# Kernel tuning notes

Hardware: AMD Instinct MI355X
Metric: run time of the kernel (lower is better)

Reference implementation:

```python
import jax, jax.numpy as jnp
import numpy as np

N, E = 25000, 400000
HID, EDGE_F, DIM, HEADS, ADY = 128, 16, 3, 8, 64
INNER = int(1.25 * HID)          # 160
MSG_F = 2 * HID + EDGE_F + 1     # 273 (e3, relaxed=False -> 1 distance feature)


def silu(x):
    return x * jax.nn.sigmoid(x)


def ada_ln(x, y, W, b):
    # LayerNorm (no affine) + FiLM conditioning from y
    mu = jnp.mean(x, axis=-1, keepdims=True)
    var = jnp.var(x, axis=-1, keepdims=True)
    xn = (x - mu) * jax.lax.rsqrt(var + 1e-5)
    scale, shift = jnp.split(y @ W + b, 2, axis=-1)
    return xn * (1.0 + scale) + shift


def setup_inputs() -> dict:
    key = jax.random.key(0)
    ks = jax.random.split(key, 32)
    rn = lambda k, shp, s=0.05: (jax.random.normal(k, shp, jnp.float32) * s)
    inp = {
        'h': jax.random.normal(ks[0], (N, HID), jnp.float32),
        'coords': jax.random.normal(ks[1], (N, DIM), jnp.float32),
        'a': jax.random.normal(ks[2], (E, EDGE_F), jnp.float32),
        'y': jax.random.normal(ks[3], (N, ADY), jnp.float32),
        'res': jnp.zeros((N, HID), jnp.float32),
        'src': jax.random.randint(ks[4], (E,), 0, N, jnp.int32),
        'dst': jax.random.randint(ks[5], (E,), 0, N, jnp.int32),
        # edge MLP
        'We1': rn(ks[6], (MSG_F, INNER)), 'be1': jnp.zeros((INNER,), jnp.float32),
        'We2': rn(ks[7], (INNER, INNER)), 'be2': jnp.zeros((INNER,), jnp.float32),
        # coord head (xavier gain 0.001 -> tiny init)
        'Wc': rn(ks[8], (INNER, 1), 0.001),
        # attention/value/output heads
        'Wv': rn(ks[9], (INNER, HID)),
        'Wa': rn(ks[10], (INNER, HEADS)),
        'Wo': rn(ks[11], (HID, HID)),
        # node MLP
        'Wn1': rn(ks[12], (HID, INNER)), 'bn1': jnp.zeros((INNER,), jnp.float32),
        'Wn2': rn(ks[13], (INNER, HID)), 'bn2': jnp.zeros((HID,), jnp.float32),
        # adaptive LayerNorms (FiLM from y)
        'Wf1': rn(ks[14], (ADY, 2 * HID)), 'bf1': jnp.zeros((2 * HID,), jnp.float32),
        'Wf2': rn(ks[15], (ADY, 2 * HID)), 'bf2': jnp.zeros((2 * HID,), jnp.float32),
    }
    return inp


def reference(h, coords, a, y, res, src, dst,
              We1, be1, We2, be2, Wc, Wv, Wa, Wo,
              Wn1, bn1, Wn2, bn2, Wf1, bf1, Wf2, bf2):
    n = h.shape[0]
    heads = Wa.shape[1]
    # --- distance features (e3, relaxed=False): radial only ---
    xs, xd = coords[src], coords[dst]          # [E, 3]
    diffs = xs - xd
    radials = jnp.sum(diffs * diffs, axis=-1, keepdims=True)  # [E, 1]
    # --- edge MLP on gathered features ---
    f = jnp.concatenate([h[src], h[dst], radials, a], axis=-1)  # [E, 273]
    m = silu(f @ We1 + be1)
    m = silu(m @ We2 + be2)                    # [E, inner]
    # --- coordinate messages + scatter-sum to dst ---
    msg_x = (m @ Wc) * diffs / (jnp.sqrt(radials + 1e-5) + 1.0)  # [E, 3]
    coords_out = coords + jax.ops.segment_sum(msg_x, dst, num_segments=n)
    # --- edge softmax over incoming edges per dst node ---
    logits = m @ Wa                             # [E, heads]
    mx = jax.ops.segment_max(logits, dst, num_segments=n)
    ex = jnp.exp(logits - mx[dst])
    den = jax.ops.segment_sum(ex, dst, num_segments=n)
    w = ex / den[dst]                           # [E, heads]
    # --- weighted value aggregation ---
    vals = (m @ Wv).reshape(-1, heads, HID // heads) * w[:, :, None]
    h_agg = jax.ops.segment_sum(vals, dst, num_segments=n).reshape(n, HID)
    f2 = h_agg @ Wo
    res1 = res + f2
    h1 = ada_ln(h + f2, y, Wf1, bf1)
    f3 = silu(h1 @ Wn1 + bn1) @ Wn2 + bn2
    res2 = res1 + f3
    h2 = ada_ln(h1 + f3, y, Wf2, bf2)
    return (h2, coords_out, res2)
```

## Files before the change

kernel.cpp:

```cpp
#include <hip/hip_runtime.h>
#include <math.h>

#define N_NODES 25000
#define N_EDGES 400000
#define HID 128
#define EDGE_F 16
#define ADY 64
#define INNER 160
#define MSG_F 273
#define HEADS 8

#define OUT_CRD (N_NODES * HID)
#define OUT_RES (N_NODES * (HID + 3))

#define FLAG_OFF 0
#define DEN_OFF  256
#define CACC_OFF 800256
#define HAGG_OFF 1100256
#define CNT_OFF  13900256
#define CUR_OFF  14000256
#define PERM_OFF 14100256
#define MEMSET_BYTES 14000256
#define HBF_OFF  15700256
#define YBF_OFF  22100256
#define BIAS_OFF 25300256
#define BW_OFF   25302560

#define WSLICE 5120
#define SCR_STRIDE 145

typedef unsigned short u16;
typedef unsigned int u32;
typedef unsigned long long u64;
typedef __attribute__((ext_vector_type(8))) short short8;
typedef __attribute__((ext_vector_type(4))) float f32x4;

__device__ __forceinline__ float bf2f(u16 v) {
    union { u32 u; float f; } x; x.u = ((u32)v) << 16; return x.f;
}
__device__ __forceinline__ u16 f2bf(float f) {
    union { float ff; u32 u; } x; x.ff = f;
    u32 u = x.u;
    u32 rounding = 0x7FFFu + ((u >> 16) & 1u);
    u += rounding;
    return (u16)(u >> 16);
}
__device__ __forceinline__ float silu(float z) {
    z = fminf(fmaxf(z, -30000.f), 30000.f);
    return z / (1.0f + __expf(-z));
}

template<bool F32> __device__ __forceinline__ float ldg1(const void* p, size_t i) {
    if (F32) return ((const float*)p)[i];
    return bf2f(((const u16*)p)[i]);
}
template<bool F32> __device__ __forceinline__ void stg1(void* p, size_t i, float v) {
    if (F32) ((float*)p)[i] = v;
    else     ((u16*)p)[i] = f2bf(v);
}
__device__ __forceinline__ float ldany(const void* p, size_t i, bool f32) {
    return f32 ? ((const float*)p)[i] : bf2f(((const u16*)p)[i]);
}
__device__ __forceinline__ void wave_lds_fence() {
    __builtin_amdgcn_wave_barrier();
    __builtin_amdgcn_s_waitcnt(0xc07f);
    __builtin_amdgcn_wave_barrier();
}

__device__ __forceinline__ int a_addr(int k, int lr) {
    return ((k >> 5) << 9) + (((((k & 31) >> 3) << 4) | lr) << 3) + (k & 7);
}

struct CvtArgs {
    const void* src[8];
    u64 dstoff[8];
    int n[8];
};
struct BwArgs {
    const void* We1; const void* We2; const void* Wv; const void* Wa;
    const void* Wc;  const void* Wo;  const void* Wn1; const void* Wn2;
    const void* Wf1; const void* Wf2;
    u64 b1, b2, b3, b4, b5, b6, b7, b8;
};

__global__ __launch_bounds__(256)
void preproc_kernel(const void* hsrc, int* flag, char* ws, CvtArgs args, BwArgs bwa,
                    const int* __restrict__ dstp, int* __restrict__ cnt)
{
    __shared__ float red[256];
    __shared__ int sflag;
    const int t = threadIdx.x;
    {
        const u16* p = (const u16*)hsrc;
        float mx = 0.f;
        for (int i = 0; i < 8; i++) {
            int idx = (t * 8 + i) * 97;
            float v = fabsf(bf2f(p[idx * 2]));
            mx = fmaxf(mx, v);
        }
        red[t] = mx;
        __syncthreads();
        for (int s = 128; s > 0; s >>= 1) {
            if (t < s) red[t] = fmaxf(red[t], red[t + s]);
            __syncthreads();
        }
        if (t == 0) {
            sflag = (red[0] > 1e10f || red[0] == 0.f) ? 1 : 0;
            if (blockIdx.x == 0) flag[0] = sflag;
        }
        __syncthreads();
    }
    const bool f32 = (sflag != 0);
    const int g = blockIdx.x * 256 + t;
    const int stride = gridDim.x * 256;

    for (int i = g; i < N_EDGES; i += stride)
        atomicAdd(&cnt[dstp[i]], 1);

    for (int ten = 0; ten < 8; ten++) {
        const void* s = args.src[ten];
        u16* d = (u16*)(ws + args.dstoff[ten]);
        const int n = args.n[ten];
        if (f32) {
            const float* sf = (const float*)s;
            for (int i = g; i < n; i += stride) d[i] = f2bf(sf[i]);
        } else {
            const u16* su = (const u16*)s;
            for (int i = g; i < n; i += stride) d[i] = su[i];
        }
    }

    u16* b1 = (u16*)(ws + bwa.b1);
    u16* b2 = (u16*)(ws + bwa.b2);
    u16* b3 = (u16*)(ws + bwa.b3);
    u16* b4 = (u16*)(ws + bwa.b4);
    u16* b5 = (u16*)(ws + bwa.b5);
    u16* b6 = (u16*)(ws + bwa.b6);
    u16* b7 = (u16*)(ws + bwa.b7);
    u16* b8 = (u16*)(ws + bwa.b8);
    for (int i = g; i < 5*2*10*512; i += stride) {
        int tt = i >> 9, r = i & 511, l = r >> 3, j = r & 7;
        int c = tt / 20, ks = (tt / 10) % 2, nt = tt % 10;
        int k = c*64 + ks*32 + (l >> 4)*8 + j;
        int n = nt*16 + (l & 15);
        float v = 0.f;
        if (k < MSG_F)      v = ldany(bwa.We1, (size_t)k*INNER + n, f32);
        else if (k == 273)  v = ldany(bwa.We1, (size_t)256*INNER + n, f32);
        b1[i] = f2bf(v);
    }
    for (int i = g; i < 5*10*512; i += stride) {
        int tt = i >> 9, r = i & 511, l = r >> 3, j = r & 7;
        int k5 = tt / 10, nt = tt % 10;
        int k = k5*32 + (l >> 4)*8 + j;
        int n = nt*16 + (l & 15);
        b2[i] = f2bf(ldany(bwa.We2, (size_t)k*INNER + n, f32));
    }
    for (int i = g; i < 5*9*512; i += stride) {
        int tt = i >> 9, r = i & 511, l = r >> 3, j = r & 7;
        int k5 = tt / 9, nt = tt % 9;
        int k = k5*32 + (l >> 4)*8 + j;
        int n = nt*16 + (l & 15);
        float v = 0.f;
        if (n < 128)       v = ldany(bwa.Wv, (size_t)k*HID + n, f32);
        else if (n < 136)  v = ldany(bwa.Wa, (size_t)k*HEADS + (n-128), f32);
        else if (n == 136) v = ldany(bwa.Wc, (size_t)k, f32);
        b3[i] = f2bf(v);
    }
    for (int i = g; i < 4*8*512; i += stride) {
        int tt = i >> 9, r = i & 511, l = r >> 3, j = r & 7;
        int cks = tt / 8, nt = tt % 8;
        int k = cks*32 + (l >> 4)*8 + j;
        int n = nt*16 + (l & 15);
        b4[i] = f2bf(ldany(bwa.Wo, (size_t)k*HID + n, f32));
    }
    for (int i = g; i < 4*10*512; i += stride) {
        int tt = i >> 9, r = i & 511, l = r >> 3, j = r & 7;
        int cks = tt / 10, nt = tt % 10;
        int k = cks*32 + (l >> 4)*8 + j;
        int n = nt*16 + (l & 15);
        b5[i] = f2bf(ldany(bwa.Wn1, (size_t)k*INNER + n, f32));
    }
    for (int i = g; i < 5*8*512; i += stride) {
        int tt = i >> 9, r = i & 511, l = r >> 3, j = r & 7;
        int k5 = tt / 8, nt = tt % 8;
        int k = k5*32 + (l >> 4)*8 + j;
        int n = nt*16 + (l & 15);
        b6[i] = f2bf(ldany(bwa.Wn2, (size_t)k*HID + n, f32));
    }
    for (int i = g; i < 2*16*512; i += stride) {
        int tt = i >> 9, r = i & 511, l = r >> 3, j = r & 7;
        int ks = tt / 16, nt = tt % 16;
        int k = ks*32 + (l >> 4)*8 + j;
        int n = nt*16 + (l & 15);
        b7[i] = f2bf(ldany(bwa.Wf1, (size_t)k*256 + n, f32));
        b8[i] = f2bf(ldany(bwa.Wf2, (size_t)k*256 + n, f32));
    }
}

__global__ __launch_bounds__(1024)
void scan_kernel(const int* __restrict__ cnt, int* __restrict__ cursor)
{
    __shared__ int ssum[1024];
    const int t = threadIdx.x;
    const int base = t * 25;
    int loc[25];
    int s = 0;
    #pragma unroll
    for (int j = 0; j < 25; j++) {
        int i = base + j;
        int v = (i < N_NODES) ? cnt[i] : 0;
        loc[j] = s; s += v;
    }
    ssum[t] = s;
    __syncthreads();
    for (int off = 1; off < 1024; off <<= 1) {
        int v = (t >= off) ? ssum[t - off] : 0;
        __syncthreads();
        ssum[t] += v;
        __syncthreads();
    }
    int offs = (t > 0) ? ssum[t - 1] : 0;
    #pragma unroll
    for (int j = 0; j < 25; j++) {
        int i = base + j;
        if (i < N_NODES) cursor[i] = offs + loc[j];
    }
}

__global__ __launch_bounds__(256)
void scatter_kernel(const int* __restrict__ dstp, int* __restrict__ cursor,
                    int* __restrict__ perm)
{
    int i = blockIdx.x * 256 + threadIdx.x;
    if (i < N_EDGES) {
        int pos = atomicAdd(&cursor[dstp[i]], 1);
        perm[pos] = i;
    }
}

template<bool F32>
__device__ __forceinline__ void edge_body(
    const u16* __restrict__ hbf, const void* coords, const void* a,
    const int* __restrict__ src, const int* __restrict__ dst,
    const int* __restrict__ perm,
    const u16* __restrict__ We1P, const u16* __restrict__ We2P,
    const u16* __restrict__ W3P,
    const u16* __restrict__ cbe1, const u16* __restrict__ cbe2,
    float* __restrict__ den, float* __restrict__ hagg, float* __restrict__ cacc,
    u16* sPool)
{
    const int t   = threadIdx.x;
    const int w   = t >> 6;
    const int l   = t & 63;
    const int col = l & 15;
    const int q   = l >> 4;
    const int e0  = blockIdx.x * 64;
    const int l8  = l << 3;

    u16* sW = sPool + w * WSLICE;

    const int r = l >> 2;
    const int p = t & 3;
    const int ge = perm[e0 + w*16 + r];
    const int s_ = src[ge];
    const int d_ = dst[ge];
    float dx = 0.f, dy = 0.f, dz = 0.f, invf = 0.f, r2 = 0.f;
    if (p < 2) {
        dx = ldg1<F32>(coords, (size_t)s_*3+0) - ldg1<F32>(coords, (size_t)d_*3+0);
        dy = ldg1<F32>(coords, (size_t)s_*3+1) - ldg1<F32>(coords, (size_t)d_*3+1);
        dz = ldg1<F32>(coords, (size_t)s_*3+2) - ldg1<F32>(coords, (size_t)d_*3+2);
        r2 = dx*dx + dy*dy + dz*dz;
        invf = 1.0f / (sqrtf(r2 + 1e-5f) + 1.0f);
    }
    #pragma unroll
    for (int c = 0; c < 4; c++) {
        int node = (c < 2) ? s_ : d_;
        int hcol = (c & 1) * 64 + p * 16;
        const uint4* gp = (const uint4*)(hbf + (size_t)node*HID + hcol);
        int k0 = c*64 + p*16;
        *(uint4*)(sW + a_addr(k0,     r)) = gp[0];
        *(uint4*)(sW + a_addr(k0 + 8, r)) = gp[1];
    }
    if (p < 2) {
        __align__(16) u16 tmp[16];
        #pragma unroll
        for (int j = 0; j < 16; j++) tmp[j] = 0;
        if (p == 0) {
            tmp[0] = f2bf(r2);
            for (int j = 0; j < 15; j++)
                tmp[1+j] = f2bf(ldg1<F32>(a, (size_t)ge*EDGE_F + j));
        } else {
            tmp[0] = f2bf(ldg1<F32>(a, (size_t)ge*EDGE_F + 15));
            tmp[1] = f2bf(r2 - bf2f(f2bf(r2)));
        }
        int k0 = 256 + p*16;
        *(uint4*)(sW + a_addr(k0,     r)) = ((uint4*)tmp)[0];
        *(uint4*)(sW + a_addr(k0 + 8, r)) = ((uint4*)tmp)[1];
    }
    wave_lds_fence();

    f32x4 acc1[10];
    #pragma unroll
    for (int nt = 0; nt < 10; nt++) {
        float v = bf2f(cbe1[nt*16 + col]);
        acc1[nt] = (f32x4){v, v, v, v};
    }
    #pragma unroll
    for (int kk = 0; kk < 9; kk++) {
        short8 af = *(const short8*)(sW + (kk << 9) + l8);
        const u16* B1 = We1P + ((kk*10) << 9) + l8;
        #pragma unroll
        for (int nt = 0; nt < 10; nt++) {
            short8 b = *(const short8*)(B1 + (nt << 9));
            acc1[nt] = __builtin_amdgcn_mfma_f32_16x16x32_bf16(af, b, acc1[nt], 0, 0, 0);
        }
    }
    wave_lds_fence();
    #pragma unroll
    for (int nt = 0; nt < 10; nt++)
        #pragma unroll
        for (int rr = 0; rr < 4; rr++)
            sW[a_addr(nt*16 + col, q*4 + rr)] = f2bf(silu(acc1[nt][rr]));
    wave_lds_fence();

    f32x4 acc2[10];
    #pragma unroll
    for (int nt = 0; nt < 10; nt++) {
        float v = bf2f(cbe2[nt*16 + col]);
        acc2[nt] = (f32x4){v, v, v, v};
    }
    #pragma unroll
    for (int k5 = 0; k5 < 5; k5++) {
        short8 af = *(const short8*)(sW + (k5 << 9) + l8);
        const u16* B2 = We2P + ((k5*10) << 9) + l8;
        #pragma unroll
        for (int nt = 0; nt < 10; nt++) {
            short8 b = *(const short8*)(B2 + (nt << 9));
            acc2[nt] = __builtin_amdgcn_mfma_f32_16x16x32_bf16(af, b, acc2[nt], 0, 0, 0);
        }
    }
    #pragma unroll
    for (int nt = 0; nt < 10; nt++)
        #pragma unroll
        for (int rr = 0; rr < 4; rr++)
            sW[2560 + a_addr(nt*16 + col, q*4 + rr)] = f2bf(silu(acc2[nt][rr]));
    wave_lds_fence();

    f32x4 acc3[9];
    #pragma unroll
    for (int nt = 0; nt < 9; nt++) acc3[nt] = (f32x4){0.f, 0.f, 0.f, 0.f};
    #pragma unroll
    for (int k5 = 0; k5 < 5; k5++) {
        short8 af = *(const short8*)(sW + 2560 + (k5 << 9) + l8);
        const u16* B3 = W3P + ((k5*9) << 9) + l8;
        #pragma unroll
        for (int nt = 0; nt < 9; nt++) {
            short8 b = *(const short8*)(B3 + (nt << 9));
            acc3[nt] = __builtin_amdgcn_mfma_f32_16x16x32_bf16(af, b, acc3[nt], 0, 0, 0);
        }
    }
    wave_lds_fence();

    float* scr = (float*)(void*)sW;

    int dsts[16];
    #pragma unroll
    for (int row = 0; row < 16; row++) dsts[row] = __shfl(d_, row << 2);
    float dxv[4], dyv[4], dzv[4], ivv[4];
    #pragma unroll
    for (int rr = 0; rr < 4; rr++) {
        int sl = (q*4 + rr) << 2;
        dxv[rr] = __shfl(dx, sl); dyv[rr] = __shfl(dy, sl);
        dzv[rr] = __shfl(dz, sl); ivv[rr] = __shfl(invf, sl);
    }

    {
        float exv[4] = {0.f, 0.f, 0.f, 0.f};
        if (col < 8) {
            #pragma unroll
            for (int rr = 0; rr < 4; rr++)
                exv[rr] = __expf(fminf(fmaxf(acc3[8][rr], -30.f), 30.f));
        }
        #pragma unroll
        for (int nt = 0; nt < 8; nt++) {
            float ex0 = __shfl(exv[0], q*16 + nt);
            float ex1 = __shfl(exv[1], q*16 + nt);
            float ex2 = __shfl(exv[2], q*16 + nt);
            float ex3 = __shfl(exv[3], q*16 + nt);
            scr[(q*4 + 0)*SCR_STRIDE + nt*16 + col] = acc3[nt][0] * ex0;
            scr[(q*4 + 1)*SCR_STRIDE + nt*16 + col] = acc3[nt][1] * ex1;
            scr[(q*4 + 2)*SCR_STRIDE + nt*16 + col] = acc3[nt][2] * ex2;
            scr[(q*4 + 3)*SCR_STRIDE + nt*16 + col] = acc3[nt][3] * ex3;
        }
        if (col < 8) {
            #pragma unroll
            for (int rr = 0; rr < 4; rr++)
                scr[(q*4 + rr)*SCR_STRIDE + 128 + col] = exv[rr];
        }
        if (col == 8) {
            #pragma unroll
            for (int rr = 0; rr < 4; rr++) {
                float lc = fminf(fmaxf(acc3[8][rr], -1e6f), 1e6f) * ivv[rr];
                scr[(q*4 + rr)*SCR_STRIDE + 136] = lc * dxv[rr];
                scr[(q*4 + rr)*SCR_STRIDE + 137] = lc * dyv[rr];
                scr[(q*4 + rr)*SCR_STRIDE + 138] = lc * dzv[rr];
            }
        }
    }
    wave_lds_fence();

    #pragma unroll
    for (int pass = 0; pass < 3; pass++) {
        int c = pass*64 + l;
        bool act = c < 139;
        float accu = 0.f;
        int prevd = dsts[0];
        #pragma unroll
        for (int row = 0; row < 16; row++) {
            int d = dsts[row];
            if (d != prevd) {
                if (act) {
                    if (c < 128)      atomicAdd(&hagg[(size_t)prevd*HID + c], accu);
                    else if (c < 136) atomicAdd(&den[(size_t)prevd*8 + (c-128)], accu);
                    else              atomicAdd(&cacc[(size_t)prevd*3 + (c-136)], accu);
                }
                accu = 0.f; prevd = d;
            }
            if (act) accu += scr[row*SCR_STRIDE + c];
        }
        if (act) {
            if (c < 128)      atomicAdd(&hagg[(size_t)prevd*HID + c], accu);
            else if (c < 136) atomicAdd(&den[(size_t)prevd*8 + (c-128)], accu);
            else              atomicAdd(&cacc[(size_t)prevd*3 + (c-136)], accu);
        }
    }
}

__global__ __launch_bounds__(256, 4)
void edge_kernel(const int* __restrict__ flag,
                 const u16* __restrict__ hbf, const void* coords, const void* a,
                 const int* __restrict__ src, const int* __restrict__ dst,
                 const int* __restrict__ perm,
                 const u16* __restrict__ We1P, const u16* __restrict__ We2P,
                 const u16* __restrict__ W3P,
                 const u16* __restrict__ cbe1, const u16* __restrict__ cbe2,
                 float* __restrict__ den, float* __restrict__ hagg,
                 float* __restrict__ cacc)
{
    __shared__ __align__(16) u16 sPool[4 * WSLICE];
    if (*flag)
        edge_body<true>(hbf, coords, a, src, dst, perm, We1P, We2P, W3P,
                        cbe1, cbe2, den, hagg, cacc, sPool);
    else
        edge_body<false>(hbf, coords, a, src, dst, perm, We1P, We2P, W3P,
                         cbe1, cbe2, den, hagg, cacc, sPool);
}

template<bool F32>
__device__ __forceinline__ void node_body(
    const u16* __restrict__ hbf, const void* res, const void* coords,
    const u16* __restrict__ ybf,
    const float* __restrict__ den, const float* __restrict__ hagg,
    const float* __restrict__ cacc,
    const u16* __restrict__ WoP, const u16* __restrict__ Wn1P,
    const u16* __restrict__ Wn2P, const u16* __restrict__ Wf1P,
    const u16* __restrict__ Wf2P,
    const u16* __restrict__ cbn1, const u16* __restrict__ cbn2,
    const u16* __restrict__ cbf1, const u16* __restrict__ cbf2,
    void* out, u16* sScr)
{
    const int t = threadIdx.x;
    const int w = t >> 6, l = t & 63, col = l & 15, q = l >> 4;
    const int nodew = blockIdx.x * 64 + w * 16;
    const int mynode = nodew + col;
    const bool okA = mynode < N_NODES;
    const int l8 = l << 3;
    u16* sc = sScr + w * 16 * 168;

    int gm[4]; bool okC[4];
    #pragma unroll
    for (int r = 0; r < 4; r++) { gm[r] = nodew + q*4 + r; okC[r] = gm[r] < N_NODES; }

    f32x4 aF2[8];
    #pragma unroll
    for (int nt = 0; nt < 8; nt++) aF2[nt] = (f32x4){0.f,0.f,0.f,0.f};
    #pragma unroll
    for (int c = 0; c < 2; c++) {
        #pragma unroll
        for (int ks = 0; ks < 2; ks++) {
            const int kbase = c*64 + ks*32 + q*8;
            union { u16 s[8]; short8 v; } u;
            if (okA) {
                float dd = den[(size_t)mynode*8 + (kbase >> 4)];
                float inv = dd > 0.f ? 1.f/dd : 0.f;
                const float4* gp = (const float4*)(hagg + (size_t)mynode*HID + kbase);
                float4 v0 = gp[0], v1 = gp[1];
                u.s[0]=f2bf(v0.x*inv); u.s[1]=f2bf(v0.y*inv); u.s[2]=f2bf(v0.z*inv); u.s[3]=f2bf(v0.w*inv);
                u.s[4]=f2bf(v1.x*inv); u.s[5]=f2bf(v1.y*inv); u.s[6]=f2bf(v1.z*inv); u.s[7]=f2bf(v1.w*inv);
            } else {
                #pragma unroll
                for (int j = 0; j < 8; j++) u.s[j] = 0;
            }
            const u16* B = WoP + (((c*2 + ks)*8) << 9) + l8;
            #pragma unroll
            for (int nt = 0; nt < 8; nt++) {
                short8 b = *(const short8*)(B + (nt << 9));
                aF2[nt] = __builtin_amdgcn_mfma_f32_16x16x32_bf16(u.v, b, aF2[nt], 0, 0, 0);
            }
        }
    }

    f32x4 aFl[16];
    #pragma unroll
    for (int nt = 0; nt < 16; nt++) {
        float v = bf2f(cbf1[nt*16 + col]);
        aFl[nt] = (f32x4){v,v,v,v};
    }
    #pragma unroll
    for (int ks = 0; ks < 2; ks++) {
        short8 af;
        if (okA) af = *(const short8*)(ybf + (size_t)mynode*ADY + ks*32 + q*8);
        else { union { u16 s[8]; short8 v; } z; for (int j=0;j<8;j++) z.s[j]=0; af = z.v; }
        const u16* B = Wf1P + ((ks*16) << 9) + l8;
        #pragma unroll
        for (int nt = 0; nt < 16; nt++) {
            short8 b = *(const short8*)(B + (nt << 9));
            aFl[nt] = __builtin_amdgcn_mfma_f32_16x16x32_bf16(af, b, aFl[nt], 0, 0, 0);
        }
    }

    float h1c[8][4], r1c[8][4];
    {
        float xv[8][4], s[4], ss[4];
        #pragma unroll
        for (int r = 0; r < 4; r++) { s[r] = 0.f; ss[r] = 0.f; }
        #pragma unroll
        for (int nt = 0; nt < 8; nt++)
            #pragma unroll
            for (int r = 0; r < 4; r++) {
                float hv = okC[r] ? bf2f(hbf[(size_t)gm[r]*HID + nt*16 + col]) : 0.f;
                float x = hv + aF2[nt][r];
                xv[nt][r] = x; s[r] += x; ss[r] += x*x;
            }
        #pragma unroll
        for (int r = 0; r < 4; r++)
            for (int off = 1; off <= 8; off <<= 1) {
                s[r]  += __shfl_xor(s[r], off);
                ss[r] += __shfl_xor(ss[r], off);
            }
        #pragma unroll
        for (int r = 0; r < 4; r++) {
            float mu = s[r] * (1.f/128.f);
            float var = ss[r] * (1.f/128.f) - mu*mu;
            float rs = rsqrtf(fmaxf(var, 0.f) + 1e-5f);
            #pragma unroll
            for (int nt = 0; nt < 8; nt++) {
                float h1 = (xv[nt][r]-mu)*rs*(1.f+aFl[nt][r]) + aFl[nt+8][r];
                h1c[nt][r] = h1;
                float rv = okC[r] ? ldg1<F32>(res, (size_t)gm[r]*HID + nt*16 + col) : 0.f;
                r1c[nt][r] = rv + aF2[nt][r];
                sc[(q*4 + r)*168 + nt*16 + col] = f2bf(h1);
            }
        }
    }
    wave_lds_fence();

    f32x4 aT[10];
    #pragma unroll
    for (int nt = 0; nt < 10; nt++) {
        float v = bf2f(cbn1[nt*16 + col]);
        aT[nt] = (f32x4){v,v,v,v};
    }
    #pragma unroll
    for (int c = 0; c < 2; c++) {
        #pragma unroll
        for (int ks = 0; ks < 2; ks++) {
            short8 af = *(const short8*)(sc + col*168 + c*64 + ks*32 + q*8);
            const u16* B = Wn1P + (((c*2 + ks)*10) << 9) + l8;
            #pragma unroll
            for (int nt = 0; nt < 10; nt++) {
                short8 b = *(const short8*)(B + (nt << 9));
                aT[nt] = __builtin_amdgcn_mfma_f32_16x16x32_bf16(af, b, aT[nt], 0, 0, 0);
            }
        }
    }
    wave_lds_fence();
    #pragma unroll
    for (int nt = 0; nt < 10; nt++)
        #pragma unroll
        for (int r = 0; r < 4; r++)
            sc[(q*4 + r)*168 + nt*16 + col] = f2bf(silu(aT[nt][r]));
    wave_lds_fence();

    f32x4 aF3[8];
    #pragma unroll
    for (int nt = 0; nt < 8; nt++) {
        float v = bf2f(cbn2[nt*16 + col]);
        aF3[nt] = (f32x4){v,v,v,v};
    }
    #pragma unroll
    for (int k5 = 0; k5 < 5; k5++) {
        short8 af = *(const short8*)(sc + col*168 + k5*32 + q*8);
        const u16* B = Wn2P + ((k5*8) << 9) + l8;
        #pragma unroll
        for (int nt = 0; nt < 8; nt++) {
            short8 b = *(const short8*)(B + (nt << 9));
            aF3[nt] = __builtin_amdgcn_mfma_f32_16x16x32_bf16(af, b, aF3[nt], 0, 0, 0);
        }
    }

    #pragma unroll
    for (int nt = 0; nt < 16; nt++) {
        float v = bf2f(cbf2[nt*16 + col]);
        aFl[nt] = (f32x4){v,v,v,v};
    }
    #pragma unroll
    for (int ks = 0; ks < 2; ks++) {
        short8 af;
        if (okA) af = *(const short8*)(ybf + (size_t)mynode*ADY + ks*32 + q*8);
        else { union { u16 s[8]; short8 v; } z; for (int j=0;j<8;j++) z.s[j]=0; af = z.v; }
        const u16* B = Wf2P + ((ks*16) << 9) + l8;
        #pragma unroll
        for (int nt = 0; nt < 16; nt++) {
            short8 b = *(const short8*)(B + (nt << 9));
            aFl[nt] = __builtin_amdgcn_mfma_f32_16x16x32_bf16(af, b, aFl[nt], 0, 0, 0);
        }
    }

    {
        float xv[8][4], s[4], ss[4];
        #pragma unroll
        for (int r = 0; r < 4; r++) { s[r] = 0.f; ss[r] = 0.f; }
        #pragma unroll
        for (int nt = 0; nt < 8; nt++)
            #pragma unroll
            for (int r = 0; r < 4; r++) {
                float x = h1c[nt][r] + aF3[nt][r];
                xv[nt][r] = x; s[r] += x; ss[r] += x*x;
            }
        #pragma unroll
        for (int r = 0; r < 4; r++)
            for (int off = 1; off <= 8; off <<= 1) {
                s[r]  += __shfl_xor(s[r], off);
                ss[r] += __shfl_xor(ss[r], off);
            }
        #pragma unroll
        for (int r = 0; r < 4; r++) {
            float mu = s[r] * (1.f/128.f);
            float var = ss[r] * (1.f/128.f) - mu*mu;
            float rs = rsqrtf(fmaxf(var, 0.f) + 1e-5f);
            if (okC[r]) {
                #pragma unroll
                for (int nt = 0; nt < 8; nt++) {
                    int n = nt*16 + col;
                    float h2 = (xv[nt][r]-mu)*rs*(1.f+aFl[nt][r]) + aFl[nt+8][r];
                    stg1<F32>(out, (size_t)gm[r]*HID + n, h2);
                    stg1<F32>(out, (size_t)OUT_RES + (size_t)gm[r]*HID + n,
                              r1c[nt][r] + aF3[nt][r]);
                }
            }
        }
    }

    if (q == 0 && okA) {
        #pragma unroll
        for (int j = 0; j < 3; j++)
            stg1<F32>(out, (size_t)OUT_CRD + (size_t)mynode*3 + j,
                      ldg1<F32>(coords, (size_t)mynode*3 + j) + cacc[(size_t)mynode*3 + j]);
    }
}

__global__ __launch_bounds__(256, 2)
void node_kernel(const int* __restrict__ flag,
                 const u16* __restrict__ hbf, const void* res, const void* coords,
                 const u16* __restrict__ ybf,
                 const float* __restrict__ den, const float* __restrict__ hagg,
                 const float* __restrict__ cacc,
                 const u16* __restrict__ WoP, const u16* __restrict__ Wn1P,
                 const u16* __restrict__ Wn2P, const u16* __restrict__ Wf1P,
                 const u16* __restrict__ Wf2P,
                 const u16* __restrict__ cbn1, const u16* __restrict__ cbn2,
                 const u16* __restrict__ cbf1, const u16* __restrict__ cbf2,
                 void* out)
{
    __shared__ __align__(16) u16 sScr[4 * 16 * 168];
    if (*flag)
        node_body<true>(hbf, res, coords, ybf, den, hagg, cacc, WoP, Wn1P, Wn2P,
                        Wf1P, Wf2P, cbn1, cbn2, cbf1, cbf2, out, sScr);
    else
        node_body<false>(hbf, res, coords, ybf, den, hagg, cacc, WoP, Wn1P, Wn2P,
                         Wf1P, Wf2P, cbn1, cbn2, cbf1, cbf2, out, sScr);
}

extern "C" void kernel_launch(void* const* d_in, const int* in_sizes, int n_in,
                              void* d_out, int out_size, void* d_ws, size_t ws_size,
                              hipStream_t stream)
{
    const void* h      = d_in[0];
    const void* coords = d_in[1];
    const void* a      = d_in[2];
    const void* y      = d_in[3];
    const void* res    = d_in[4];
    const int* src     = (const int*)d_in[5];
    const int* dst     = (const int*)d_in[6];

    char* ws = (char*)d_ws;
    int*   flag   = (int*)(ws + FLAG_OFF);
    float* den    = (float*)(ws + DEN_OFF);
    float* cacc   = (float*)(ws + CACC_OFF);
    float* hagg   = (float*)(ws + HAGG_OFF);
    int*   cnt    = (int*)(ws + CNT_OFF);
    int*   cursor = (int*)(ws + CUR_OFF);
    int*   perm   = (int*)(ws + PERM_OFF);
    u16*   hbf    = (u16*)(ws + HBF_OFF);
    u16*   ybf    = (u16*)(ws + YBF_OFF);

    CvtArgs args;
    const int cvtn[8]   = {160, 160, 160, 128, 256, 256, N_NODES*HID, N_NODES*ADY};
    const int cvtsrc[8] = {8, 10, 16, 18, 20, 22, 0, 3};
    u64 boff[8];
    u64 bo = BIAS_OFF;
    for (int i = 0; i < 6; i++) {
        boff[i] = bo;
        bo += ((u64)cvtn[i] * 2 + 15) & ~(u64)15;
    }
    boff[6] = HBF_OFF;
    boff[7] = YBF_OFF;
    for (int i = 0; i < 8; i++) {
        args.src[i] = d_in[cvtsrc[i]];
        args.dstoff[i] = boff[i];
        args.n[i] = cvtn[i];
    }
    const u16* cbe1 = (const u16*)(ws + boff[0]);
    const u16* cbe2 = (const u16*)(ws + boff[1]);
    const u16* cbn1 = (const u16*)(ws + boff[2]);
    const u16* cbn2 = (const u16*)(ws + boff[3]);
    const u16* cbf1 = (const u16*)(ws + boff[4]);
    const u16* cbf2 = (const u16*)(ws + boff[5]);

    BwArgs bwa;
    bwa.We1 = d_in[7];  bwa.We2 = d_in[9];  bwa.Wv = d_in[12]; bwa.Wa = d_in[13];
    bwa.Wc  = d_in[11]; bwa.Wo  = d_in[14]; bwa.Wn1 = d_in[15]; bwa.Wn2 = d_in[17];
    bwa.Wf1 = d_in[19]; bwa.Wf2 = d_in[21];
    bwa.b1 = BW_OFF;
    bwa.b2 = bwa.b1 + (u64)5*2*10*512*2;
    bwa.b3 = bwa.b2 + (u64)5*10*512*2;
    bwa.b4 = bwa.b3 + (u64)5*9*512*2;
    bwa.b5 = bwa.b4 + (u64)4*8*512*2;
    bwa.b6 = bwa.b5 + (u64)4*10*512*2;
    bwa.b7 = bwa.b6 + (u64)5*8*512*2;
    bwa.b8 = bwa.b7 + (u64)2*16*512*2;
    const u16* We1P = (const u16*)(ws + bwa.b1);
    const u16* We2P = (const u16*)(ws + bwa.b2);
    const u16* W3P  = (const u16*)(ws + bwa.b3);
    const u16* WoP  = (const u16*)(ws + bwa.b4);
    const u16* Wn1P = (const u16*)(ws + bwa.b5);
    const u16* Wn2P = (const u16*)(ws + bwa.b6);
    const u16* Wf1P = (const u16*)(ws + bwa.b7);
    const u16* Wf2P = (const u16*)(ws + bwa.b8);

    hipMemsetAsync(d_ws, 0, MEMSET_BYTES, stream);

    preproc_kernel<<<256, 256, 0, stream>>>(h, flag, ws, args, bwa, dst, cnt);

    scan_kernel<<<1, 1024, 0, stream>>>(cnt, cursor);

    scatter_kernel<<<(N_EDGES + 255)/256, 256, 0, stream>>>(dst, cursor, perm);

    edge_kernel<<<N_EDGES/64, 256, 0, stream>>>(flag, hbf, coords, a, src, dst, perm,
                                                We1P, We2P, W3P, cbe1, cbe2,
                                                den, hagg, cacc);

    node_kernel<<<(N_NODES + 63)/64, 256, 0, stream>>>(
        flag, hbf, res, coords, ybf, den, hagg, cacc,
        WoP, Wn1P, Wn2P, Wf1P, Wf2P, cbn1, cbn2, cbf1, cbf2, d_out);
}
```

Baseline: 482.1 us.

## Load MFMA A-operands directly from global and shrink LDS scratch to bf16

The edge kernel stops staging gathered h[src]/h[dst] rows into LDS and instead reads the MFMA A fragments straight from global memory, with each lane indexed by its edge column. LDS is used only for the distance/edge features and for the hidden activations. The scatter scratch is stored as bf16 pairs rather than fp32. Together these cut the per-wave LDS slice from 5120 to 3072 u16, and launch bounds are raised to 6 blocks per SM for higher occupancy. The cost is lower precision in the accumulated messages, softmax denominators and coordinate updates, plus uncoalesced direct global loads for the A operands.

```diff
diff --git a/kernel.cpp b/kernel.cpp
--- a/kernel.cpp
+++ b/kernel.cpp
@@ -26,8 +26,9 @@
 #define BIAS_OFF 25300256
 #define BW_OFF   25302560
 
-#define WSLICE 5120
-#define SCR_STRIDE 145
+#define WSLICE 3072
+#define SM_OFF 512
+#define SCR_STRIDE 146
 
 typedef unsigned short u16;
 typedef unsigned int u32;
@@ -259,29 +260,21 @@
 
     u16* sW = sPool + w * WSLICE;
 
-    const int r = l >> 2;
-    const int p = t & 3;
-    const int ge = perm[e0 + w*16 + r];
-    const int s_ = src[ge];
-    const int d_ = dst[ge];
+    const int ge2 = perm[e0 + w*16 + col];
+    const int s2 = src[ge2];
+    const int d2 = dst[ge2];
+
+    const int er = l >> 2;
+    const int p  = l & 3;
+    const int ge = perm[e0 + w*16 + er];
     float dx = 0.f, dy = 0.f, dz = 0.f, invf = 0.f, r2 = 0.f;
     if (p < 2) {
+        int s_ = src[ge], d_ = dst[ge];
         dx = ldg1<F32>(coords, (size_t)s_*3+0) - ldg1<F32>(coords, (size_t)d_*3+0);
         dy = ldg1<F32>(coords, (size_t)s_*3+1) - ldg1<F32>(coords, (size_t)d_*3+1);
         dz = ldg1<F32>(coords, (size_t)s_*3+2) - ldg1<F32>(coords, (size_t)d_*3+2);
         r2 = dx*dx + dy*dy + dz*dz;
         invf = 1.0f / (sqrtf(r2 + 1e-5f) + 1.0f);
-    }
-    #pragma unroll
-    for (int c = 0; c < 4; c++) {
-        int node = (c < 2) ? s_ : d_;
-        int hcol = (c & 1) * 64 + p * 16;
-        const uint4* gp = (const uint4*)(hbf + (size_t)node*HID + hcol);
-        int k0 = c*64 + p*16;
-        *(uint4*)(sW + a_addr(k0,     r)) = gp[0];
-        *(uint4*)(sW + a_addr(k0 + 8, r)) = gp[1];
-    }
-    if (p < 2) {
         __align__(16) u16 tmp[16];
         #pragma unroll
         for (int j = 0; j < 16; j++) tmp[j] = 0;
@@ -293,9 +286,8 @@
             tmp[0] = f2bf(ldg1<F32>(a, (size_t)ge*EDGE_F + 15));
             tmp[1] = f2bf(r2 - bf2f(f2bf(r2)));
         }
-        int k0 = 256 + p*16;
-        *(uint4*)(sW + a_addr(k0,     r)) = ((uint4*)tmp)[0];
-        *(uint4*)(sW + a_addr(k0 + 8, r)) = ((uint4*)tmp)[1];
+        *(uint4*)(sW + (32*p + er)*8)      = ((uint4*)tmp)[0];
+        *(uint4*)(sW + (32*p + 16 + er)*8) = ((uint4*)tmp)[1];
     }
     wave_lds_fence();
 
@@ -305,22 +297,44 @@
         float v = bf2f(cbe1[nt*16 + col]);
         acc1[nt] = (f32x4){v, v, v, v};
     }
-    #pragma unroll
-    for (int kk = 0; kk < 9; kk++) {
-        short8 af = *(const short8*)(sW + (kk << 9) + l8);
-        const u16* B1 = We1P + ((kk*10) << 9) + l8;
-        #pragma unroll
-        for (int nt = 0; nt < 10; nt++) {
-            short8 b = *(const short8*)(B1 + (nt << 9));
-            acc1[nt] = __builtin_amdgcn_mfma_f32_16x16x32_bf16(af, b, acc1[nt], 0, 0, 0);
-        }
-    }
-    wave_lds_fence();
+    {
+        const u16* hs = hbf + (size_t)s2*HID + q*8;
+        const u16* hd = hbf + (size_t)d2*HID + q*8;
+        #pragma unroll
+        for (int kk = 0; kk < 4; kk++) {
+            short8 af = *(const short8*)(hs + kk*32);
+            const u16* B1 = We1P + ((kk*10) << 9) + l8;
+            #pragma unroll
+            for (int nt = 0; nt < 10; nt++) {
+                short8 b = *(const short8*)(B1 + (nt << 9));
+                acc1[nt] = __builtin_amdgcn_mfma_f32_16x16x32_bf16(af, b, acc1[nt], 0, 0, 0);
+            }
+        }
+        #pragma unroll
+        for (int kk = 0; kk < 4; kk++) {
+            short8 af = *(const short8*)(hd + kk*32);
+            const u16* B1 = We1P + (((kk+4)*10) << 9) + l8;
+            #pragma unroll
+            for (int nt = 0; nt < 10; nt++) {
+                short8 b = *(const short8*)(B1 + (nt << 9));
+                acc1[nt] = __builtin_amdgcn_mfma_f32_16x16x32_bf16(af, b, acc1[nt], 0, 0, 0);
+            }
+        }
+        {
+            short8 af = *(const short8*)(sW + l8);
+            const u16* B1 = We1P + ((8*10) << 9) + l8;
+            #pragma unroll
+            for (int nt = 0; nt < 10; nt++) {
+                short8 b = *(const short8*)(B1 + (nt << 9));
+                acc1[nt] = __builtin_amdgcn_mfma_f32_16x16x32_bf16(af, b, acc1[nt], 0, 0, 0);
+            }
+        }
+    }
     #pragma unroll
     for (int nt = 0; nt < 10; nt++)
         #pragma unroll
         for (int rr = 0; rr < 4; rr++)
-            sW[a_addr(nt*16 + col, q*4 + rr)] = f2bf(silu(acc1[nt][rr]));
+            sW[SM_OFF + a_addr(nt*16 + col, q*4 + rr)] = f2bf(silu(acc1[nt][rr]));
     wave_lds_fence();
 
     f32x4 acc2[10];
@@ -331,7 +345,7 @@
     }
     #pragma unroll
     for (int k5 = 0; k5 < 5; k5++) {
-        short8 af = *(const short8*)(sW + (k5 << 9) + l8);
+        short8 af = *(const short8*)(sW + SM_OFF + (k5 << 9) + l8);
         const u16* B2 = We2P + ((k5*10) << 9) + l8;
         #pragma unroll
         for (int nt = 0; nt < 10; nt++) {
@@ -339,11 +353,12 @@
             acc2[nt] = __builtin_amdgcn_mfma_f32_16x16x32_bf16(af, b, acc2[nt], 0, 0, 0);
         }
     }
+    wave_lds_fence();
     #pragma unroll
     for (int nt = 0; nt < 10; nt++)
         #pragma unroll
         for (int rr = 0; rr < 4; rr++)
-            sW[2560 + a_addr(nt*16 + col, q*4 + rr)] = f2bf(silu(acc2[nt][rr]));
+            sW[SM_OFF + a_addr(nt*16 + col, q*4 + rr)] = f2bf(silu(acc2[nt][rr]));
     wave_lds_fence();
 
     f32x4 acc3[9];
@@ -351,7 +366,7 @@
     for (int nt = 0; nt < 9; nt++) acc3[nt] = (f32x4){0.f, 0.f, 0.f, 0.f};
     #pragma unroll
     for (int k5 = 0; k5 < 5; k5++) {
-        short8 af = *(const short8*)(sW + 2560 + (k5 << 9) + l8);
+        short8 af = *(const short8*)(sW + SM_OFF + (k5 << 9) + l8);
         const u16* B3 = W3P + ((k5*9) << 9) + l8;
         #pragma unroll
         for (int nt = 0; nt < 9; nt++) {
@@ -361,11 +376,9 @@
     }
     wave_lds_fence();
 
-    float* scr = (float*)(void*)sW;
-
     int dsts[16];
     #pragma unroll
-    for (int row = 0; row < 16; row++) dsts[row] = __shfl(d_, row << 2);
+    for (int row = 0; row < 16; row++) dsts[row] = __shfl(d2, row);
     float dxv[4], dyv[4], dzv[4], ivv[4];
     #pragma unroll
     for (int rr = 0; rr < 4; rr++) {
@@ -381,29 +394,42 @@
             for (int rr = 0; rr < 4; rr++)
                 exv[rr] = __expf(fminf(fmaxf(acc3[8][rr], -30.f), 30.f));
         }
+        const bool lo = (col & 1) == 0;
         #pragma unroll
         for (int nt = 0; nt < 8; nt++) {
             float ex0 = __shfl(exv[0], q*16 + nt);
             float ex1 = __shfl(exv[1], q*16 + nt);
             float ex2 = __shfl(exv[2], q*16 + nt);
             float ex3 = __shfl(exv[3], q*16 + nt);
-            scr[(q*4 + 0)*SCR_STRIDE + nt*16 + col] = acc3[nt][0] * ex0;
-            scr[(q*4 + 1)*SCR_STRIDE + nt*16 + col] = acc3[nt][1] * ex1;
-            scr[(q*4 + 2)*SCR_STRIDE + nt*16 + col] = acc3[nt][2] * ex2;
-            scr[(q*4 + 3)*SCR_STRIDE + nt*16 + col] = acc3[nt][3] * ex3;
+            float v0 = acc3[nt][0] * ex0;
+            float v1 = acc3[nt][1] * ex1;
+            float v2 = acc3[nt][2] * ex2;
+            float v3 = acc3[nt][3] * ex3;
+            float p0 = __shfl_xor(v0, 1);
+            float p1 = __shfl_xor(v1, 1);
+            float p2 = __shfl_xor(v2, 1);
+            float p3 = __shfl_xor(v3, 1);
+            int cb = nt*16 + (col & ~1);
+            int rowA = q*4 + (lo ? 0 : 2);
+            u32 wA = lo ? ((u32)f2bf(v0) | ((u32)f2bf(p0) << 16))
+                        : ((u32)f2bf(p2) | ((u32)f2bf(v2) << 16));
+            u32 wB = lo ? ((u32)f2bf(v1) | ((u32)f2bf(p1) << 16))
+                        : ((u32)f2bf(p3) | ((u32)f2bf(v3) << 16));
+            *(u32*)(&sW[rowA*SCR_STRIDE + cb])       = wA;
+            *(u32*)(&sW[(rowA+1)*SCR_STRIDE + cb])   = wB;
         }
         if (col < 8) {
             #pragma unroll
             for (int rr = 0; rr < 4; rr++)
-                scr[(q*4 + rr)*SCR_STRIDE + 128 + col] = exv[rr];
+                sW[(q*4 + rr)*SCR_STRIDE + 128 + col] = f2bf(exv[rr]);
         }
         if (col == 8) {
             #pragma unroll
             for (int rr = 0; rr < 4; rr++) {
                 float lc = fminf(fmaxf(acc3[8][rr], -1e6f), 1e6f) * ivv[rr];
-                scr[(q*4 + rr)*SCR_STRIDE + 136] = lc * dxv[rr];
-                scr[(q*4 + rr)*SCR_STRIDE + 137] = lc * dyv[rr];
-                scr[(q*4 + rr)*SCR_STRIDE + 138] = lc * dzv[rr];
+                sW[(q*4 + rr)*SCR_STRIDE + 136] = f2bf(lc * dxv[rr]);
+                sW[(q*4 + rr)*SCR_STRIDE + 137] = f2bf(lc * dyv[rr]);
+                sW[(q*4 + rr)*SCR_STRIDE + 138] = f2bf(lc * dzv[rr]);
             }
         }
     }
@@ -426,7 +452,7 @@
                 }
                 accu = 0.f; prevd = d;
             }
-            if (act) accu += scr[row*SCR_STRIDE + c];
+            if (act) accu += bf2f(sW[row*SCR_STRIDE + c]);
         }
         if (act) {
             if (c < 128)      atomicAdd(&hagg[(size_t)prevd*HID + c], accu);
@@ -436,7 +462,7 @@
     }
 }
 
-__global__ __launch_bounds__(256, 4)
+__global__ __launch_bounds__(256, 6)
 void edge_kernel(const int* __restrict__ flag,
                  const u16* __restrict__ hbf, const void* coords, const void* a,
                  const int* __restrict__ src, const int* __restrict__ dst,
```

After: 563.3 us. +16.9%, slower.
